# Performance work log

Hardware: AMD Instinct MI355X
Metric: run time of the kernel (lower is better)

Reference implementation:

```python
import jax, jax.numpy as jnp
from jax import lax
import numpy as np
import math

B, LBL, PRED, CIN = 16, 48, 336, 7
L = LBL + PRED
DM, E = 512, 2
DIN, N, DCONV = 2 * DM, 16, 4
DTR = math.ceil(DM / 16)  # 32
TF = 4  # freq='h' time features
EPS = 1e-5


def _ln(x, w, b):
    m = x.mean(-1, keepdims=True)
    v = ((x - m) ** 2).mean(-1, keepdims=True)
    return (x - m) / jnp.sqrt(v + EPS) * w + b


def _silu(x):
    return x * jax.nn.sigmoid(x)


def _token_embed(x, w):
    # Conv1d(c_in, d_model, k=3, padding=1, circular, bias=False). x: (B,L,C), w: (DM,C,3)
    xp = jnp.concatenate([x[:, -1:], x, x[:, :1]], axis=1)  # circular pad along L
    y = lax.conv_general_dilated(xp.transpose(0, 2, 1), w, (1,), 'VALID',
                                 dimension_numbers=('NCH', 'OIH', 'NCH'))
    return y.transpose(0, 2, 1)  # (B,L,DM)


def _selective_scan(u, dt, A, Bm, Cm):
    # u,dt: (B,L,DIN); A: (DIN,N); Bm,Cm: (B,L,N)
    h0 = jnp.zeros((u.shape[0], DIN, N), u.dtype)

    def step(h, inp):
        u_t, dt_t, B_t, C_t = inp  # (B,DIN),(B,DIN),(B,N),(B,N)
        dA = jnp.exp(dt_t[:, :, None] * A)  # (B,DIN,N)
        h = dA * h + (dt_t * u_t)[:, :, None] * B_t[:, None, :]
        y = jnp.einsum('bdn,bn->bd', h, C_t)
        return h, y

    _, ys = lax.scan(step, h0, (u.transpose(1, 0, 2), dt.transpose(1, 0, 2),
                                Bm.transpose(1, 0, 2), Cm.transpose(1, 0, 2)))
    return ys.transpose(1, 0, 2)  # (B,L,DIN)


def _mamba(x, p):
    (in_w, conv_w, conv_b, xproj_w, dtproj_w, dtproj_b, A_log, Dp, out_w) = p
    xz = x @ in_w.T                      # (B,L,2*DIN)
    xin, z = jnp.split(xz, 2, axis=-1)
    # depthwise causal conv1d, kernel DCONV
    xt = jnp.pad(xin.transpose(0, 2, 1), ((0, 0), (0, 0), (DCONV - 1, 0)))
    xc = lax.conv_general_dilated(xt, conv_w, (1,), 'VALID', feature_group_count=DIN,
                                  dimension_numbers=('NCH', 'OIH', 'NCH'))
    xc = _silu((xc + conv_b[None, :, None]).transpose(0, 2, 1))  # (B,L,DIN)
    dbc = xc @ xproj_w.T                 # (B,L,DTR+2N)
    dt_r, Bm, Cm = dbc[..., :DTR], dbc[..., DTR:DTR + N], dbc[..., DTR + N:]
    dt = jax.nn.softplus(dt_r @ dtproj_w.T + dtproj_b)  # (B,L,DIN)
    A = -jnp.exp(A_log)                  # (DIN,N)
    y = _selective_scan(xc, dt, A, Bm, Cm) + xc * Dp
    y = y * _silu(z)
    return y @ out_w.T                   # (B,L,DM)


def _model(x_dec, x_mark_dec, token_w, timef_w, layer_ps, fin_w, fin_b, out_w):
    mean = lax.stop_gradient(x_dec[:, :LBL].mean(1, keepdims=True))
    head = x_dec[:, :LBL] - mean
    std = lax.stop_gradient(jnp.sqrt(head.var(axis=1, keepdims=True) + EPS))
    head = head / std
    xd = jnp.concatenate([head, x_dec[:, LBL:]], axis=1)
    x = _token_embed(xd, token_w) + x_mark_dec @ timef_w.T  # DataEmbedding_wo_pos (eval: no dropout)
    for i in range(E):
        nw, nb = layer_ps[0][i], layer_ps[1][i]
        mp = tuple(layer_ps[j][i] for j in range(2, 11))
        x = x + _mamba(_ln(x, nw, nb), mp)
    x = _ln(x, fin_w, fin_b)
    out = x @ out_w.T
    out = out * std + mean
    return out[:, -PRED:, :]


def setup_inputs() -> dict:
    key = jax.random.key(0)
    ks = jax.random.split(key, 20)
    s = 0.02
    d = {
        'x_enc': jax.random.normal(ks[0], (B, 96, CIN), jnp.float32),
        'x_mark_enc': jax.random.normal(ks[1], (B, 96, TF), jnp.float32),
        'x_dec': jax.random.normal(ks[2], (B, L, CIN), jnp.float32),
        'x_mark_dec': jax.random.normal(ks[3], (B, L, TF), jnp.float32),
        'token_w': jax.random.normal(ks[4], (DM, CIN, 3), jnp.float32) * s,
        'timef_w': jax.random.normal(ks[5], (DM, TF), jnp.float32) * s,
        'norm_w': jnp.ones((E, DM), jnp.float32),
        'norm_b': jnp.zeros((E, DM), jnp.float32),
        'in_proj_w': jax.random.normal(ks[6], (E, 2 * DIN, DM), jnp.float32) * s,
        'conv_w': jax.random.normal(ks[7], (E, DIN, 1, DCONV), jnp.float32) * s,
        'conv_b': jnp.zeros((E, DIN), jnp.float32),
        'xproj_w': jax.random.normal(ks[8], (E, DTR + 2 * N, DIN), jnp.float32) * s,
        'dtproj_w': jax.random.normal(ks[9], (E, DIN, DTR), jnp.float32) * s,
        'dtproj_b': jnp.full((E, DIN), -4.0, jnp.float32),
        'A_log': jnp.tile(jnp.log(jnp.arange(1, N + 1, dtype=jnp.float32)), (E, DIN, 1)),
        'D': jnp.ones((E, DIN), jnp.float32),
        'outproj_w': jax.random.normal(ks[10], (E, DM, DIN), jnp.float32) * s,
        'final_norm_w': jnp.ones((DM,), jnp.float32),
        'final_norm_b': jnp.zeros((DM,), jnp.float32),
        'out_w': jax.random.normal(ks[11], (CIN, DM), jnp.float32) * s,
    }
    return d


def reference(x_enc, x_mark_enc, x_dec, x_mark_dec, token_w, timef_w, norm_w, norm_b,
              in_proj_w, conv_w, conv_b, xproj_w, dtproj_w, dtproj_b, A_log, D,
              outproj_w, final_norm_w, final_norm_b, out_w):
    layer_ps = (norm_w, norm_b, in_proj_w, conv_w, conv_b, xproj_w, dtproj_w,
                dtproj_b, A_log, D, outproj_w)
    return _model(x_dec, x_mark_dec, token_w, timef_w, layer_ps,
                  final_norm_w, final_norm_b, out_w)
```

## Files before the change

### kernel.cpp

```cpp
#include <hip/hip_runtime.h>

#define B_    16
#define LBL_  48
#define PRED_ 336
#define CIN_  7
#define L_    384
#define DM_   512
#define E_    2
#define DIN_  1024
#define N_    16
#define DCONV_ 4
#define DTR_  32
#define TF_   4
#define EPSF  1e-5f
#define NSEG  16
#define SEGL  24
#define SC2   2
#define NCHK  12

typedef unsigned short u16;
typedef __attribute__((ext_vector_type(8))) short short8;
typedef __attribute__((ext_vector_type(4))) float f32x4;

__device__ __forceinline__ float bf2f(u16 u){
  union { float f; unsigned int i; } cv; cv.i = ((unsigned int)u) << 16; return cv.f;
}
__device__ __forceinline__ u16 f2bf(float f){
  union { float f; unsigned int i; } cv; cv.f = f;
  unsigned int x = cv.i;
  unsigned int lsb = (x >> 16) & 1u;
  x += 0x7fffu + lsb;
  return (u16)(x >> 16);
}
__device__ __forceinline__ float lo16(unsigned int v){
  union { float f; unsigned int i; } cv; cv.i = v << 16; return cv.f;
}
__device__ __forceinline__ float hi16(unsigned int v){
  union { float f; unsigned int i; } cv; cv.i = v & 0xffff0000u; return cv.f;
}

#define GLDS(g, l) __builtin_amdgcn_global_load_lds( \
    (const __attribute__((address_space(1))) void*)(g), \
    (__attribute__((address_space(3))) void*)(l), 16, 0, 0)

#define PO_XDEC   0
#define PO_XMARK  43008
#define PO_TOKW   67584
#define PO_TIMEF  78336
#define PO_NORMW  80384
#define PO_NORMB  81408
#define PO_INW    82432
#define PO_CONVW  2179584
#define PO_CONVB  2187776
#define PO_XPROJ  2189824
#define PO_DTW    2320896
#define PO_DTB    2386432
#define PO_ALOG   2388480
#define PO_DP     2421248
#define PO_OUTW   2423296
#define PO_FNW    3471872
#define PO_FNB    3472384
#define PO_HEADW  3472896
#define P_TOTAL   3476480
#define A_X    3476480
#define A_LNB  6622208
#define A_XZ   9767936
#define A_DT   22350848
#define A_DBC  28642304
#define A_XD   29035520
#define A_MEAN 29078528
#define A_STD  29078640
#define A_DBC4 16059392
#define DBC_SL ((size_t)(B_*L_)*64)

struct Ptrs { const void* p[18]; };

__device__ __forceinline__ float wredsum(float s){
  #pragma unroll
  for (int off = 32; off; off >>= 1) s += __shfl_xor(s, off, 64);
  return s;
}

__device__ __forceinline__ void qpowers(float q, float* p){
  float q2 = q*q;
  float q4 = q2*q2;
  float q8 = q4*q4;
  float q3 = q2*q;
  p[0]=q;      p[1]=q2;     p[2]=q3;     p[3]=q4;
  p[4]=q4*q;   p[5]=q4*q2;  p[6]=q4*q3;  p[7]=q8;
  p[8]=q8*q;   p[9]=q8*q2;  p[10]=q8*q3; p[11]=q8*q4;
  p[12]=q8*p[4]; p[13]=q8*p[5]; p[14]=q8*p[6]; p[15]=q8*q8;
}

__device__ __forceinline__ unsigned int xcd_swz(unsigned int bid, unsigned int nwg){
  return (bid & 7u) * (nwg >> 3) + (bid >> 3);
}

__global__ __launch_bounds__(256) void convert_kernel(Ptrs ps, float* __restrict__ dst){
  const int offs[18] = {PO_XDEC, PO_XMARK, PO_TOKW, PO_TIMEF, PO_NORMW, PO_NORMB,
                        PO_INW, PO_CONVW, PO_CONVB, PO_XPROJ, PO_DTW, PO_DTB,
                        PO_ALOG, PO_DP, PO_OUTW, PO_FNW, PO_FNB, PO_HEADW};
  int idx = blockIdx.x * 256 + threadIdx.x;
  if (idx >= P_TOTAL) return;
  int seg = 0;
  #pragma unroll
  for (int s = 1; s < 18; s++) if (idx >= offs[s]) seg = s;
  int off = idx - offs[seg];
  int isbf = (((const u16*)ps.p[4])[0] == 0x3F80u);
  if (seg == 6 || seg == 9 || seg == 10 || seg == 14){
    u16 hv = isbf ? ((const u16*)ps.p[seg])[off]
                  : f2bf(((const float*)ps.p[seg])[off]);
    ((u16*)(dst + offs[seg]))[off] = hv;
  } else {
    float v = isbf ? bf2f(((const u16*)ps.p[seg])[off])
                   : ((const float*)ps.p[seg])[off];
    dst[idx] = v;
  }
}

__global__ __launch_bounds__(64) void prep_kernel(const float* __restrict__ x_dec, float* __restrict__ xd,
                            float* __restrict__ meanv, float* __restrict__ stdv){
  int i = blockIdx.x;
  int b = i / CIN_, c = i % CIN_;
  int lane = threadIdx.x;
  float v0 = (lane < LBL_) ? x_dec[(b*L_+lane)*CIN_+c] : 0.f;
  float m = wredsum(v0) * (1.f/LBL_);
  float dv = (lane < LBL_) ? (v0 - m) : 0.f;
  float sd = sqrtf(wredsum(dv*dv) * (1.f/LBL_) + EPSF);
  if (lane == 0){ meanv[i] = m; stdv[i] = sd; }
  float inv = 1.f / sd;
  #pragma unroll
  for (int t = lane; t < L_; t += 64){
    float v = x_dec[(b*L_+t)*CIN_+c];
    xd[(b*L_+t)*CIN_+c] = (t < LBL_) ? (v - m) * inv : v;
  }
}

__global__ __launch_bounds__(256) void embed_ln_kernel(const float* __restrict__ xd,
      const float* __restrict__ token_w, const float* __restrict__ x_mark,
      const float* __restrict__ timef_w, const float* __restrict__ nw,
      const float* __restrict__ nb, float* __restrict__ x, u16* __restrict__ out){
  int tok = blockIdx.x*4 + (threadIdx.x >> 6);
  int lane = threadIdx.x & 63;
  int t = tok % L_;
  int b = tok / L_;
  int tm1 = (t == 0) ? L_-1 : t-1;
  int tp1 = (t == L_-1) ? 0 : t+1;
  const float* r0 = xd + (b*L_+tm1)*CIN_;
  const float* r1 = xd + (b*L_+t  )*CIN_;
  const float* r2 = xd + (b*L_+tp1)*CIN_;
  const float* mk = x_mark + (b*L_+t)*TF_;
  float a0[CIN_], a1[CIN_], a2[CIN_], mkv[TF_];
  #pragma unroll
  for (int ci = 0; ci < CIN_; ci++){ a0[ci]=r0[ci]; a1[ci]=r1[ci]; a2[ci]=r2[ci]; }
  #pragma unroll
  for (int f = 0; f < TF_; f++) mkv[f] = mk[f];
  float v[8];
  #pragma unroll
  for (int j = 0; j < 8; j++){
    int d = lane*8 + j;
    float acc = 0.f;
    #pragma unroll
    for (int ci = 0; ci < CIN_; ci++){
      const float* w = token_w + (d*CIN_+ci)*3;
      acc += a0[ci]*w[0] + a1[ci]*w[1] + a2[ci]*w[2];
    }
    #pragma unroll
    for (int f = 0; f < TF_; f++)
      acc += mkv[f] * timef_w[d*TF_+f];
    v[j] = acc;
  }
  float* xr = x + (size_t)tok*DM_ + lane*8;
  *(float4*)xr       = (float4){v[0],v[1],v[2],v[3]};
  *(float4*)(xr + 4) = (float4){v[4],v[5],v[6],v[7]};
  float s = (v[0]+v[1])+(v[2]+v[3])+((v[4]+v[5])+(v[6]+v[7]));
  float mean = wredsum(s) * (1.f/DM_);
  float s2 = 0.f;
  #pragma unroll
  for (int j = 0; j < 8; j++){ v[j] -= mean; s2 += v[j]*v[j]; }
  float rstd = rsqrtf(wredsum(s2) * (1.f/DM_) + EPSF);
  const float* wr = nw + lane*8;
  const float* br = nb + lane*8;
  uint4 o; unsigned int* op = (unsigned int*)&o;
  #pragma unroll
  for (int k = 0; k < 4; k++){
    u16 e0 = f2bf(v[2*k]   * rstd * wr[2*k]   + br[2*k]);
    u16 e1 = f2bf(v[2*k+1] * rstd * wr[2*k+1] + br[2*k+1]);
    op[k] = (unsigned int)e0 | ((unsigned int)e1 << 16);
  }
  *(uint4*)(out + (size_t)tok*DM_ + lane*8) = o;
}

__global__ __launch_bounds__(256) void ln_kernel(const float* __restrict__ x,
     const float* __restrict__ w, const float* __restrict__ bias, u16* __restrict__ out){
  int tok = blockIdx.x*4 + (threadIdx.x >> 6);
  int lane = threadIdx.x & 63;
  const float* xr = x + (size_t)tok*DM_ + lane*8;
  float4 a = *(const float4*)xr;
  float4 bq = *(const float4*)(xr + 4);
  float v[8] = {a.x,a.y,a.z,a.w,bq.x,bq.y,bq.z,bq.w};
  float s = (v[0]+v[1])+(v[2]+v[3])+((v[4]+v[5])+(v[6]+v[7]));
  float mean = wredsum(s) * (1.f/DM_);
  float s2 = 0.f;
  #pragma unroll
  for (int j = 0; j < 8; j++){ v[j] -= mean; s2 += v[j]*v[j]; }
  float rstd = rsqrtf(wredsum(s2) * (1.f/DM_) + EPSF);
  const float* wr = w + lane*8;
  const float* br = bias + lane*8;
  uint4 o; unsigned int* op = (unsigned int*)&o;
  #pragma unroll
  for (int k = 0; k < 4; k++){
    u16 e0 = f2bf(v[2*k]   * rstd * wr[2*k]   + br[2*k]);
    u16 e1 = f2bf(v[2*k+1] * rstd * wr[2*k+1] + br[2*k+1]);
    op[k] = (unsigned int)e0 | ((unsigned int)e1 << 16);
  }
  *(uint4*)(out + (size_t)tok*DM_ + lane*8) = o;
}

template<int TN, int ACCUM, int BF16OUT>
__global__ __launch_bounds__(256) void gemm_mfma(const u16* __restrict__ A, const u16* __restrict__ Wt,
    void* __restrict__ C, int M, int N, int K){
  constexpr int WN = TN / 2;
  constexpr int NI = WN / 16;
  __shared__ u16 As[128 * 64];
  __shared__ u16 Ws[TN * 64];
  int tid = threadIdx.x;
  int wv = tid >> 6, lane = tid & 63;
  int wm = (wv & 1) * 64, wn = (wv >> 1) * WN;
  unsigned int gx = gridDim.x;
  unsigned int bid = blockIdx.y * gx + blockIdx.x;
  unsigned int swz = xcd_swz(bid, gx * gridDim.y);
  int m0 = (int)(swz / gx) * 128, n0 = (int)(swz % gx) * TN;
  int la = lane & 15, lk = lane >> 4;
  f32x4 acc[4][NI];
  #pragma unroll
  for (int i = 0; i < 4; i++)
    #pragma unroll
    for (int j = 0; j < NI; j++) acc[i][j] = (f32x4){0.f, 0.f, 0.f, 0.f};
  int sr = lane >> 3;
  int sc = (((lane & 7) ^ (sr & 7)) * 8);
  const u16* Ag = A + (size_t)(m0 + wv*32 + sr) * K + sc;
  u16* Al = As + (wv*32)*64 + lane*8;
  const u16 *Wg; u16 *Wl;
  if constexpr (TN == 128){
    Wg = Wt + (size_t)(n0 + wv*32 + sr) * K + sc;
    Wl = Ws + (wv*32)*64 + lane*8;
  } else {
    Wg = Wt + (size_t)(n0 + wv*16 + sr) * K + sc;
    Wl = Ws + (wv*16)*64 + lane*8;
  }
  for (int k0 = 0; k0 < K; k0 += 64){
    #pragma unroll
    for (int i = 0; i < 4; i++) GLDS(Ag + (size_t)(i*8)*K + k0, Al + i*512);
    if constexpr (TN == 128){
      #pragma unroll
      for (int i = 0; i < 4; i++) GLDS(Wg + (size_t)(i*8)*K + k0, Wl + i*512);
    } else {
      #pragma unroll
      for (int i = 0; i < 2; i++) GLDS(Wg + (size_t)(i*8)*K + k0, Wl + i*512);
    }
    __syncthreads();
    #pragma unroll
    for (int ks = 0; ks < 2; ks++){
      short8 af[4], bfr[NI];
      int ch = (ks*4 + lk) ^ (la & 7);
      #pragma unroll
      for (int mi = 0; mi < 4; mi++) af[mi] = *(const short8*)&As[(wm + mi*16 + la)*64 + ch*8];
      #pragma unroll
      for (int ni = 0; ni < NI; ni++) bfr[ni] = *(const short8*)&Ws[(wn + ni*16 + la)*64 + ch*8];
      #pragma unroll
      for (int mi = 0; mi < 4; mi++)
        #pragma unroll
        for (int ni = 0; ni < NI; ni++)
          acc[mi][ni] = __builtin_amdgcn_mfma_f32_16x16x32_bf16(af[mi], bfr[ni], acc[mi][ni], 0, 0, 0);
    }
    __syncthreads();
  }
  #pragma unroll
  for (int mi = 0; mi < 4; mi++)
    #pragma unroll
    for (int ni = 0; ni < NI; ni++){
      int row = m0 + wm + mi*16 + lk*4;
      int col = n0 + wn + ni*16 + la;
      #pragma unroll
      for (int r = 0; r < 4; r++){
        if constexpr (BF16OUT){
          u16* p = (u16*)C + (size_t)row * N + col;
          p[(size_t)r * N] = f2bf(acc[mi][ni][r]);
        } else {
          float* p = (float*)C + (size_t)row * N + col;
          if (ACCUM) p[(size_t)r * N] += acc[mi][ni][r];
          else       p[(size_t)r * N]  = acc[mi][ni][r];
        }
      }
    }
}

__global__ __launch_bounds__(256) void xproj_mfma(const u16* __restrict__ A, const u16* __restrict__ Wt,
    float* __restrict__ out4){
  __shared__ u16 As[128 * 64];
  __shared__ u16 Ws[64 * 64];
  int tid = threadIdx.x;
  int wv = tid >> 6, lane = tid & 63;
  int wm = (wv & 1) * 64, wn = (wv >> 1) * 32;
  unsigned int gx = gridDim.x;
  unsigned int bid = blockIdx.y * gx + blockIdx.x;
  unsigned int swz = xcd_swz(bid, gx * gridDim.y);
  int m0 = (int)(swz / gx) * 128;
  int kc = (int)(swz % gx);
  int la = lane & 15, lk = lane >> 4;
  f32x4 acc[4][2];
  #pragma unroll
  for (int i = 0; i < 4; i++){ acc[i][0] = (f32x4){0.f,0.f,0.f,0.f}; acc[i][1] = (f32x4){0.f,0.f,0.f,0.f}; }
  int sr = lane >> 3;
  int sc = (((lane & 7) ^ (sr & 7)) * 8);
  const u16* Ag = A + (size_t)(m0 + wv*32 + sr) * DIN_ + kc*256 + sc;
  u16* Al = As + (wv*32)*64 + lane*8;
  const u16* Wg = Wt + (size_t)(wv*16 + sr) * DIN_ + kc*256 + sc;
  u16* Wl = Ws + (wv*16)*64 + lane*8;
  for (int k0 = 0; k0 < 256; k0 += 64){
    #pragma unroll
    for (int i = 0; i < 4; i++) GLDS(Ag + (size_t)(i*8)*DIN_ + k0, Al + i*512);
    #pragma unroll
    for (int i = 0; i < 2; i++) GLDS(Wg + (size_t)(i*8)*DIN_ + k0, Wl + i*512);
    __syncthreads();
    #pragma unroll
    for (int ks = 0; ks < 2; ks++){
      short8 af[4], bfr[2];
      int ch = (ks*4 + lk) ^ (la & 7);
      #pragma unroll
      for (int mi = 0; mi < 4; mi++) af[mi] = *(const short8*)&As[(wm + mi*16 + la)*64 + ch*8];
      #pragma unroll
      for (int ni = 0; ni < 2; ni++) bfr[ni] = *(const short8*)&Ws[(wn + ni*16 + la)*64 + ch*8];
      #pragma unroll
      for (int mi = 0; mi < 4; mi++)
        #pragma unroll
        for (int ni = 0; ni < 2; ni++)
          acc[mi][ni] = __builtin_amdgcn_mfma_f32_16x16x32_bf16(af[mi], bfr[ni], acc[mi][ni], 0, 0, 0);
    }
    __syncthreads();
  }
  #pragma unroll
  for (int mi = 0; mi < 4; mi++)
    #pragma unroll
    for (int ni = 0; ni < 2; ni++){
      int row = m0 + wm + mi*16 + lk*4;
      int col = wn + ni*16 + la;
      #pragma unroll
      for (int r = 0; r < 4; r++)
        out4[((size_t)kc*(B_*L_) + row + r)*64 + col] = acc[mi][ni][r];
    }
}

__global__ __launch_bounds__(256) void dtproj_mfma(const float* __restrict__ dbc4,
    const u16* __restrict__ dtwb, const float* __restrict__ dtb, u16* __restrict__ dt){
  __shared__ u16 As[128 * 32];
  __shared__ u16 Ws[64 * 32];
  int tid = threadIdx.x;
  int wv = tid >> 6, lane = tid & 63;
  int wm = (wv & 1) * 64, wn = (wv >> 1) * 32;
  unsigned int gx = gridDim.x;
  unsigned int bid = blockIdx.y * gx + blockIdx.x;
  unsigned int swz = xcd_swz(bid, gx * gridDim.y);
  int m0 = (int)(swz / gx) * 128, n0 = (int)(swz % gx) * 64;
  int la = lane & 15, lk = lane >> 4;
  int srow = lane >> 2, scol = (lane & 3) * 8;
  #pragma unroll
  for (int i = 0; i < 8; i++){
    int idx = i*512 + tid*2;
    int row = idx >> 5, col = idx & 31;
    const float* p = dbc4 + (size_t)(m0 + row)*64 + col;
    float s0 = 0.f, s1 = 0.f;
    #pragma unroll
    for (int k = 0; k < 4; k++){
      s0 += p[(size_t)k*DBC_SL];
      s1 += p[(size_t)k*DBC_SL + 1];
    }
    *(unsigned int*)&As[row*32 + col] = (unsigned int)f2bf(s0) | ((unsigned int)f2bf(s1) << 16);
  }
  GLDS(dtwb + (size_t)(n0 + wv*16 + srow)*32 + scol, Ws + wv*512 + lane*8);
  __syncthreads();
  short8 af[4], bfr[2];
  #pragma unroll
  for (int mi = 0; mi < 4; mi++) af[mi] = *(const short8*)&As[(wm + mi*16 + la)*32 + lk*8];
  #pragma unroll
  for (int ni = 0; ni < 2; ni++) bfr[ni] = *(const short8*)&Ws[(wn + ni*16 + la)*32 + lk*8];
  #pragma unroll
  for (int mi = 0; mi < 4; mi++)
    #pragma unroll
    for (int ni = 0; ni < 2; ni++){
      f32x4 acc = (f32x4){0.f,0.f,0.f,0.f};
      acc = __builtin_amdgcn_mfma_f32_16x16x32_bf16(af[mi], bfr[ni], acc, 0, 0, 0);
      int row = m0 + wm + mi*16 + lk*4;
      int d   = n0 + wn + ni*16 + la;
      float bias = dtb[d];
      #pragma unroll
      for (int r = 0; r < 4; r++){
        float raw = acc[r] + bias;
        float sp = (raw > 20.f) ? raw : log1pf(__expf(raw));
        dt[(size_t)(row + r)*DIN_ + d] = f2bf(sp);
      }
    }
}

__global__ __launch_bounds__(256) void conv_silu_kernel(const u16* __restrict__ xz,
   const float* __restrict__ cw, const float* __restrict__ cb, u16* __restrict__ xcb){
  int e = blockIdx.x * 256 + threadIdx.x;
  int c8 = (e & (DIN_/8 - 1)) * 8;
  int bt = e >> 7;
  int t  = bt % L_;
  const u16* base = xz + (size_t)bt * (2*DIN_) + c8;
  uint4 tap[4];
  tap[3] = *(const uint4*)base;
  if (t >= 1) tap[2] = *(const uint4*)(base - 1*2*DIN_);
  if (t >= 2) tap[1] = *(const uint4*)(base - 2*2*DIN_);
  if (t >= 3) tap[0] = *(const uint4*)(base - 3*2*DIN_);
  float v[8];
  #pragma unroll
  for (int k = 0; k < 8; k++){
    float4 w = *(const float4*)(cw + (c8 + k)*4);
    float s = cb[c8 + k];
    #pragma unroll
    for (int j = 0; j < 4; j++){
      if (j >= 3 - t){
        const unsigned int* tp = (const unsigned int*)&tap[j];
        float xv = (k & 1) ? hi16(tp[k >> 1]) : lo16(tp[k >> 1]);
        s += xv * ((const float*)&w)[j];
      }
    }
    v[k] = s / (1.f + __expf(-s));
  }
  uint4 o;
  unsigned int* op = (unsigned int*)&o;
  #pragma unroll
  for (int k = 0; k < 4; k++)
    op[k] = (unsigned int)f2bf(v[2*k]) | ((unsigned int)f2bf(v[2*k+1]) << 16);
  *(uint4*)(xcb + (size_t)bt * DIN_ + c8) = o;
}

#define WSTR2 896
__global__ __launch_bounds__(1024, 1) void scan_kernel(
    u16* __restrict__ ub_yb,
    const float* __restrict__ dbc, const u16* __restrict__ xz,
    const u16* __restrict__ dtp,
    const float* __restrict__ A_log, const float* __restrict__ Dp){
  __shared__ float smem[16384];

  int tid = threadIdx.x;
  int lane = tid & 63;
  int seg  = tid >> 6;
  int b = blockIdx.x >> 4;
  int g = blockIdx.x & 15;
  int d = g*64 + lane;
  size_t base = (size_t)b * L_;

  float* wbase = smem + seg * WSTR2;
  float* sbc = wbase;
  float* su  = wbase + 128;
  float* sz  = wbase + 384;
  float* sdt = wbase + 640;

  int st = lane >> 5;
  int j  = lane & 31;

  float A[16];
  #pragma unroll
  for (int n = 0; n < 16; n += 4){
    float4 av = *(const float4*)(A_log + (size_t)d*N_ + n);
    A[n] = -__expf(av.x); A[n+1] = -__expf(av.y); A[n+2] = -__expf(av.z); A[n+3] = -__expf(av.w);
  }
  float Dv = Dp[d];
  bool fastA = true;
  #pragma unroll
  for (int n = 0; n < 16; n++) fastA = fastA && (fabsf(A[n] + (float)(n+1)) < 1e-3f*(n+1));

  float h[16];
  #pragma unroll
  for (int n = 0; n < 16; n++) h[n] = 0.f;

  auto ldc = [&](int c, float& kbc, unsigned int& ku, unsigned int& kz,
                 unsigned int& kt, bool wz){
    size_t tokr = base + seg*SEGL + c*SC2 + st;
    const float* pb = dbc + tokr*64 + 32 + j;
    kbc = (pb[0] + pb[DBC_SL]) + (pb[2*DBC_SL] + pb[3*DBC_SL]);
    ku  = ((const unsigned int*)(ub_yb + tokr*DIN_ + g*64))[j];
    kt  = ((const unsigned int*)(dtp + tokr*DIN_ + g*64))[j];
    if (wz) kz = ((const unsigned int*)(xz + tokr*(2*DIN_) + DIN_ + g*64))[j];
  };
  auto stc = [&](int buf, float kbc, unsigned int ku, unsigned int kz,
                 unsigned int kt, bool wz){
    sbc[buf*64 + st*32 + j] = kbc;
    su [buf*128 + st*64 + 2*j]     = lo16(ku);
    su [buf*128 + st*64 + 2*j + 1] = hi16(ku);
    sdt[buf*128 + st*64 + 2*j]     = lo16(kt);
    sdt[buf*128 + st*64 + 2*j + 1] = hi16(kt);
    if (wz){
      sz[buf*128 + st*64 + 2*j]     = lo16(kz);
      sz[buf*128 + st*64 + 2*j + 1] = hi16(kz);
    }
  };

  float S = 0.f;
  {
    float kbc; unsigned int ku, kz, kt;
    ldc(0, kbc, ku, kz, kt, false);
    stc(0, kbc, ku, kz, kt, false);
    for (int c = 0; c < NCHK; c++){
      int cur = c & 1;
      bool have = (c + 1 < NCHK);
      float nbc; unsigned int nu, nz, nt;
      if (have) ldc(c+1, nbc, nu, nz, nt, false);
      for (int s = 0; s < SC2; s++){
        float dtv = sdt[cur*128 + s*64 + lane];
        float u   = su [cur*128 + s*64 + lane];
        const float* bcrow = sbc + cur*64 + s*32;
        float Bf[16];
        #pragma unroll
        for (int i = 0; i < 16; i += 4){
          float4 bv = *(const float4*)(bcrow + i);
          Bf[i] = bv.x; Bf[i+1] = bv.y; Bf[i+2] = bv.z; Bf[i+3] = bv.w;
        }
        float du = dtv * u;
        S += dtv;
        if (fastA){
          float q = __expf(-dtv);
          float p[16];
          qpowers(q, p);
          #pragma unroll
          for (int n = 0; n < 16; n++) h[n] = p[n] * h[n] + du * Bf[n];
        } else {
          #pragma unroll
          for (int n = 0; n < 16; n++){
            float dA = __expf(dtv * A[n]);
            h[n] = dA * h[n] + du * Bf[n];
          }
        }
      }
      if (have) stc(1 - cur, nbc, nu, nz, nt, false);
    }
  }

  #pragma unroll
  for (int half = 0; half < 2; half++){
    __syncthreads();
    #pragma unroll
    for (int n = 0; n < 8; n++){
      int nn = half*8 + n;
      smem[(n*NSEG + seg)*64 + lane]        = h[nn];
      smem[8192 + (n*NSEG + seg)*64 + lane] = __expf(A[nn] * S);
    }
    __syncthreads();
    float hs[8];
    #pragma unroll
    for (int n = 0; n < 8; n++) hs[n] = 0.f;
    for (int jj = 0; jj < seg; jj++){
      #pragma unroll
      for (int n = 0; n < 8; n++){
        float qh = smem[(n*NSEG + jj)*64 + lane];
        float qP = smem[8192 + (n*NSEG + jj)*64 + lane];
        hs[n] = qh + qP * hs[n];
      }
    }
    #pragma unroll
    for (int n = 0; n < 8; n++) h[half*8 + n] = hs[n];
  }
  __syncthreads();

  {
    float kbc; unsigned int ku, kz, kt;
    ldc(0, kbc, ku, kz, kt, true);
    stc(0, kbc, ku, kz, kt, true);
    for (int c = 0; c < NCHK; c++){
      int cur = c & 1;
      bool have = (c + 1 < NCHK);
      float nbc; unsigned int nu, nz, nt;
      if (have) ldc(c+1, nbc, nu, nz, nt, true);
      for (int s = 0; s < SC2; s++){
        float dtv = sdt[cur*128 + s*64 + lane];
        float u   = su [cur*128 + s*64 + lane];
        float z   = sz [cur*128 + s*64 + lane];
        const float* bcrow = sbc + cur*64 + s*32;
        float Bf[16], Cf[16];
        #pragma unroll
        for (int i = 0; i < 16; i += 4){
          float4 bv = *(const float4*)(bcrow + i);
          float4 cv = *(const float4*)(bcrow + 16 + i);
          Bf[i] = bv.x; Bf[i+1] = bv.y; Bf[i+2] = bv.z; Bf[i+3] = bv.w;
          Cf[i] = cv.x; Cf[i+1] = cv.y; Cf[i+2] = cv.z; Cf[i+3] = cv.w;
        }
        float du = dtv * u;
        float acc = 0.f;
        if (fastA){
          float q = __expf(-dtv);
          float p[16];
          qpowers(q, p);
          #pragma unroll
          for (int n = 0; n < 16; n++){
            h[n] = p[n] * h[n] + du * Bf[n];
            acc += h[n] * Cf[n];
          }
        } else {
          #pragma unroll
          for (int n = 0; n < 16; n++){
            float dA = __expf(dtv * A[n]);
            h[n] = dA * h[n] + du * Bf[n];
            acc += h[n] * Cf[n];
          }
        }
        float y = acc + u * Dv;
        size_t tok = base + seg*SEGL + c*SC2 + s;
        ub_yb[tok*DIN_ + d] = f2bf(y * (z / (1.f + __expf(-z))));
      }
      if (have) stc(1 - cur, nbc, nu, nz, nt, true);
    }
  }
}

__global__ __launch_bounds__(256) void head_kernel(const float* __restrict__ x,
    const float* __restrict__ fw, const float* __restrict__ fb, const float* __restrict__ ow,
    const float* __restrict__ meanv, const float* __restrict__ stdv, void* __restrict__ out,
    const u16* __restrict__ dtype_probe){
  int wav = blockIdx.x*4 + (threadIdx.x >> 6);
  int lane = threadIdx.x & 63;
  if (wav >= B_*PRED_) return;
  int b = wav / PRED_;
  int tt = wav % PRED_;
  int tok = b*L_ + LBL_ + tt;
  const float* xr = x + (size_t)tok*DM_ + lane*8;
  float4 a = *(const float4*)xr;
  float4 bq = *(const float4*)(xr + 4);
  float v[8] = {a.x,a.y,a.z,a.w,bq.x,bq.y,bq.z,bq.w};
  float s = (v[0]+v[1])+(v[2]+v[3])+((v[4]+v[5])+(v[6]+v[7]));
  float mean = wredsum(s) * (1.f/DM_);
  float s2 = 0.f;
  #pragma unroll
  for (int j = 0; j < 8; j++){ v[j] -= mean; s2 += v[j]*v[j]; }
  float rstd = rsqrtf(wredsum(s2) * (1.f/DM_) + EPSF);
  const float* fwr = fw + lane*8;
  const float* fbr = fb + lane*8;
  #pragma unroll
  for (int j = 0; j < 8; j++) v[j] = v[j] * rstd * fwr[j] + fbr[j];
  int isbf = (dtype_probe[0] == 0x3F80u);
  for (int o = 0; o < CIN_; o++){
    const float* owr = ow + (size_t)o*DM_ + lane*8;
    float part = 0.f;
    #pragma unroll
    for (int j = 0; j < 8; j++) part += v[j] * owr[j];
    part = wredsum(part);
    if (lane == 0){
      float res = part * stdv[b*CIN_ + o] + meanv[b*CIN_ + o];
      size_t oidx = (size_t)(b*PRED_ + tt)*CIN_ + o;
      if (isbf) ((u16*)out)[oidx] = f2bf(res);
      else      ((float*)out)[oidx] = res;
    }
  }
}

extern "C" void kernel_launch(void* const* d_in, const int* in_sizes, int n_in,
                              void* d_out, int out_size, void* d_ws, size_t ws_size,
                              hipStream_t stream){
  float* P = (float*)d_ws;

  Ptrs ps;
  for (int i = 0; i < 18; i++) ps.p[i] = d_in[2 + i];

  float* x    = P + A_X;
  u16*   lnxb = (u16*)(P + A_LNB);
  u16*   xcb  = (u16*)(P + A_LNB);
  u16*   xz   = (u16*)(P + A_XZ);
  u16*   dt   = (u16*)(P + A_DT);
  float* dbc4 = P + A_DBC4;
  float* xd   = P + A_XD;
  float* meanv= P + A_MEAN;
  float* stdv = P + A_STD;
  const u16* bwi = (const u16*)(P + PO_INW);
  const u16* bwx = (const u16*)(P + PO_XPROJ);
  const u16* bwd = (const u16*)(P + PO_DTW);
  const u16* bwo = (const u16*)(P + PO_OUTW);

  convert_kernel<<<(P_TOTAL+255)/256, 256, 0, stream>>>(ps, P);
  prep_kernel<<<B_*CIN_, 64, 0, stream>>>(P + PO_XDEC, xd, meanv, stdv);
  embed_ln_kernel<<<(B_*L_)/4, 256, 0, stream>>>(
      xd, P + PO_TOKW, P + PO_XMARK, P + PO_TIMEF,
      P + PO_NORMW, P + PO_NORMB, x, lnxb);

  for (int e = 0; e < E_; e++){
    if (e > 0)
      ln_kernel<<<(B_*L_)/4, 256, 0, stream>>>(x, P + PO_NORMW + e*DM_, P + PO_NORMB + e*DM_, lnxb);
    gemm_mfma<128,0,1><<<dim3((2*DIN_)/128, (B_*L_)/128), 256, 0, stream>>>(
        lnxb, bwi + (size_t)e*2*DIN_*DM_, xz, B_*L_, 2*DIN_, DM_);
    conv_silu_kernel<<<(B_*L_*DIN_)/(256*8), 256, 0, stream>>>(
        xz, P + PO_CONVW + e*DIN_*DCONV_, P + PO_CONVB + e*DIN_, xcb);
    xproj_mfma<<<dim3(4, (B_*L_)/128), 256, 0, stream>>>(
        xcb, bwx + (size_t)e*64*DIN_, dbc4);
    dtproj_mfma<<<dim3(DIN_/64, (B_*L_)/128), 256, 0, stream>>>(
        dbc4, bwd + (size_t)e*DIN_*DTR_, P + PO_DTB + e*DIN_, dt);
    scan_kernel<<<256, 1024, 0, stream>>>(
        xcb, dbc4, xz, dt, P + PO_ALOG + e*DIN_*N_, P + PO_DP + e*DIN_);
    gemm_mfma<64,1,0><<<dim3(DM_/64, (B_*L_)/128), 256, 0, stream>>>(
        xcb, bwo + (size_t)e*DM_*DIN_, x, B_*L_, DM_, DIN_);
  }

  head_kernel<<<(B_*PRED_+3)/4, 256, 0, stream>>>(
      x, P + PO_FNW, P + PO_FNB, P + PO_HEADW, meanv, stdv, d_out, (const u16*)d_in[6]);
}
```

Measured before the change: 414.2 us.

## Fuse in-projection GEMM with causal conv+SiLU and fold prep into embed

Replaces the in_proj GEMM and the separate depthwise conv+SiLU kernel with one kernel. Each block computes a full 384-token by 64-column tile for one batch, stages the bf16 result in LDS and applies the causal conv and SiLU there. The xc half is written straight to xcb and never round-trips through xz. The input-normalisation prep kernel is folded into the embedding kernel, removing a launch and the xd buffer. The trade-offs are a larger LDS tile with lower grid parallelism (512 blocks), redundant per-block statistics computation, and xcb moving into the dt region of the workspace.

```diff
diff --git a/kernel.cpp b/kernel.cpp
--- a/kernel.cpp
+++ b/kernel.cpp
@@ -67,11 +67,11 @@
 #define A_XZ   9767936
 #define A_DT   22350848
 #define A_DBC  28642304
-#define A_XD   29035520
 #define A_MEAN 29078528
 #define A_STD  29078640
 #define A_DBC4 16059392
 #define DBC_SL ((size_t)(B_*L_)*64)
+#define A_XCB_OFF 3145728
 
 struct Ptrs { const void* p[18]; };
 
@@ -118,41 +118,39 @@
   }
 }
 
-__global__ __launch_bounds__(64) void prep_kernel(const float* __restrict__ x_dec, float* __restrict__ xd,
-                            float* __restrict__ meanv, float* __restrict__ stdv){
-  int i = blockIdx.x;
-  int b = i / CIN_, c = i % CIN_;
-  int lane = threadIdx.x;
-  float v0 = (lane < LBL_) ? x_dec[(b*L_+lane)*CIN_+c] : 0.f;
-  float m = wredsum(v0) * (1.f/LBL_);
-  float dv = (lane < LBL_) ? (v0 - m) : 0.f;
-  float sd = sqrtf(wredsum(dv*dv) * (1.f/LBL_) + EPSF);
-  if (lane == 0){ meanv[i] = m; stdv[i] = sd; }
-  float inv = 1.f / sd;
-  #pragma unroll
-  for (int t = lane; t < L_; t += 64){
-    float v = x_dec[(b*L_+t)*CIN_+c];
-    xd[(b*L_+t)*CIN_+c] = (t < LBL_) ? (v - m) * inv : v;
-  }
-}
-
-__global__ __launch_bounds__(256) void embed_ln_kernel(const float* __restrict__ xd,
+__global__ __launch_bounds__(256) void embed_ln_kernel(const float* __restrict__ x_dec,
       const float* __restrict__ token_w, const float* __restrict__ x_mark,
       const float* __restrict__ timef_w, const float* __restrict__ nw,
-      const float* __restrict__ nb, float* __restrict__ x, u16* __restrict__ out){
-  int tok = blockIdx.x*4 + (threadIdx.x >> 6);
+      const float* __restrict__ nb, float* __restrict__ x, u16* __restrict__ out,
+      float* __restrict__ meanv, float* __restrict__ stdv){
+  __shared__ float sm[8], siv[8], ssd[8];
+  int wv = threadIdx.x >> 6;
   int lane = threadIdx.x & 63;
+  int tok = blockIdx.x*4 + wv;
   int t = tok % L_;
   int b = tok / L_;
+  for (int c = wv; c < CIN_; c += 4){
+    float v0 = (lane < LBL_) ? x_dec[(b*L_+lane)*CIN_+c] : 0.f;
+    float m = wredsum(v0) * (1.f/LBL_);
+    float dv = (lane < LBL_) ? (v0 - m) : 0.f;
+    float sd = sqrtf(wredsum(dv*dv) * (1.f/LBL_) + EPSF);
+    if (lane == 0){ sm[c] = m; siv[c] = 1.f/sd; ssd[c] = sd; }
+  }
+  __syncthreads();
+  if ((blockIdx.x % (L_/4)) == 0 && threadIdx.x < CIN_){
+    meanv[b*CIN_ + threadIdx.x] = sm[threadIdx.x];
+    stdv[b*CIN_ + threadIdx.x]  = ssd[threadIdx.x];
+  }
   int tm1 = (t == 0) ? L_-1 : t-1;
   int tp1 = (t == L_-1) ? 0 : t+1;
-  const float* r0 = xd + (b*L_+tm1)*CIN_;
-  const float* r1 = xd + (b*L_+t  )*CIN_;
-  const float* r2 = xd + (b*L_+tp1)*CIN_;
+  auto ldx = [&](int row, int c){
+    float v = x_dec[(b*L_+row)*CIN_+c];
+    return (row < LBL_) ? (v - sm[c]) * siv[c] : v;
+  };
   const float* mk = x_mark + (b*L_+t)*TF_;
   float a0[CIN_], a1[CIN_], a2[CIN_], mkv[TF_];
   #pragma unroll
-  for (int ci = 0; ci < CIN_; ci++){ a0[ci]=r0[ci]; a1[ci]=r1[ci]; a2[ci]=r2[ci]; }
+  for (int ci = 0; ci < CIN_; ci++){ a0[ci]=ldx(tm1,ci); a1[ci]=ldx(t,ci); a2[ci]=ldx(tp1,ci); }
   #pragma unroll
   for (int f = 0; f < TF_; f++) mkv[f] = mk[f];
   float v[8];
@@ -215,6 +213,111 @@
     op[k] = (unsigned int)e0 | ((unsigned int)e1 << 16);
   }
   *(uint4*)(out + (size_t)tok*DM_ + lane*8) = o;
+}
+
+__global__ __launch_bounds__(256) void inproj_conv(const u16* __restrict__ A,
+    const u16* __restrict__ Wt, const float* __restrict__ cw, const float* __restrict__ cb,
+    u16* __restrict__ xz, u16* __restrict__ xcb){
+  __shared__ u16 As[384 * 64];
+  __shared__ u16 Ws[64 * 64];
+  int tid = threadIdx.x;
+  int wv = tid >> 6, lane = tid & 63;
+  unsigned int bid = blockIdx.y * 32 + blockIdx.x;
+  unsigned int swz = xcd_swz(bid, 512);
+  int b  = (int)(swz >> 5);
+  int n0 = (int)(swz & 31) * 64;
+  int m0 = b * L_;
+  int la = lane & 15, lk = lane >> 4;
+  f32x4 acc[6][4];
+  #pragma unroll
+  for (int i = 0; i < 6; i++)
+    #pragma unroll
+    for (int j = 0; j < 4; j++) acc[i][j] = (f32x4){0.f,0.f,0.f,0.f};
+  int sr = lane >> 3;
+  int sc = (((lane & 7) ^ (sr & 7)) * 8);
+  const u16* Ag = A + (size_t)(m0 + wv*96 + sr) * DM_ + sc;
+  u16* Al = As + (wv*96)*64 + lane*8;
+  const u16* Wg = Wt + (size_t)(n0 + wv*16 + sr) * DM_ + sc;
+  u16* Wl = Ws + (wv*16)*64 + lane*8;
+  for (int k0 = 0; k0 < DM_; k0 += 64){
+    #pragma unroll
+    for (int i = 0; i < 12; i++) GLDS(Ag + (size_t)(i*8)*DM_ + k0, Al + i*512);
+    #pragma unroll
+    for (int i = 0; i < 2; i++)  GLDS(Wg + (size_t)(i*8)*DM_ + k0, Wl + i*512);
+    __syncthreads();
+    #pragma unroll
+    for (int ks = 0; ks < 2; ks++){
+      int ch = (ks*4 + lk) ^ (la & 7);
+      short8 af[6], bfr[4];
+      #pragma unroll
+      for (int mi = 0; mi < 6; mi++) af[mi] = *(const short8*)&As[(wv*96 + mi*16 + la)*64 + ch*8];
+      #pragma unroll
+      for (int ni = 0; ni < 4; ni++) bfr[ni] = *(const short8*)&Ws[(ni*16 + la)*64 + ch*8];
+      #pragma unroll
+      for (int mi = 0; mi < 6; mi++)
+        #pragma unroll
+        for (int ni = 0; ni < 4; ni++)
+          acc[mi][ni] = __builtin_amdgcn_mfma_f32_16x16x32_bf16(af[mi], bfr[ni], acc[mi][ni], 0, 0, 0);
+    }
+    __syncthreads();
+  }
+  #pragma unroll
+  for (int mi = 0; mi < 6; mi++)
+    #pragma unroll
+    for (int ni = 0; ni < 4; ni++){
+      int colc = ni*2 + (la >> 3);
+      #pragma unroll
+      for (int r = 0; r < 4; r++){
+        int row = wv*96 + mi*16 + lk*4 + r;
+        As[row*64 + ((colc ^ (row & 7))<<3) + (la & 7)] = f2bf(acc[mi][ni][r]);
+      }
+    }
+  __syncthreads();
+  int c8 = (tid & 7) * 8;
+  int tg = tid >> 3;
+  if (n0 < DIN_){
+    float4 w[8]; float bias[8];
+    #pragma unroll
+    for (int k = 0; k < 8; k++){
+      w[k] = *(const float4*)(cw + (n0 + c8 + k)*4);
+      bias[k] = cb[n0 + c8 + k];
+    }
+    for (int i = 0; i < 12; i++){
+      int t = tg*12 + i;
+      uint4 tap[4];
+      #pragma unroll
+      for (int j = 0; j < 4; j++){
+        int rr = t - 3 + j;
+        if (rr >= 0)
+          tap[j] = *(const uint4*)&As[rr*64 + ((((c8>>3) ^ (rr & 7)))<<3)];
+      }
+      float v[8];
+      #pragma unroll
+      for (int k = 0; k < 8; k++){
+        float s = bias[k];
+        #pragma unroll
+        for (int j = 0; j < 4; j++){
+          if (j >= 3 - t){
+            const unsigned int* tp = (const unsigned int*)&tap[j];
+            float xv = (k & 1) ? hi16(tp[k >> 1]) : lo16(tp[k >> 1]);
+            s += xv * ((const float*)&w[k])[j];
+          }
+        }
+        v[k] = s / (1.f + __expf(-s));
+      }
+      uint4 o; unsigned int* op = (unsigned int*)&o;
+      #pragma unroll
+      for (int k = 0; k < 4; k++)
+        op[k] = (unsigned int)f2bf(v[2*k]) | ((unsigned int)f2bf(v[2*k+1]) << 16);
+      *(uint4*)(xcb + (size_t)(m0 + t)*DIN_ + n0 + c8) = o;
+    }
+  } else {
+    for (int i = 0; i < 12; i++){
+      int t = tg*12 + i;
+      uint4 vq = *(const uint4*)&As[t*64 + ((((c8>>3) ^ (t & 7)))<<3)];
+      *(uint4*)(xz + (size_t)(m0 + t)*(2*DIN_) + n0 + c8) = vq;
+    }
+  }
 }
 
 template<int TN, int ACCUM, int BF16OUT>
@@ -401,41 +504,6 @@
         dt[(size_t)(row + r)*DIN_ + d] = f2bf(sp);
       }
     }
-}
-
-__global__ __launch_bounds__(256) void conv_silu_kernel(const u16* __restrict__ xz,
-   const float* __restrict__ cw, const float* __restrict__ cb, u16* __restrict__ xcb){
-  int e = blockIdx.x * 256 + threadIdx.x;
-  int c8 = (e & (DIN_/8 - 1)) * 8;
-  int bt = e >> 7;
-  int t  = bt % L_;
-  const u16* base = xz + (size_t)bt * (2*DIN_) + c8;
-  uint4 tap[4];
-  tap[3] = *(const uint4*)base;
-  if (t >= 1) tap[2] = *(const uint4*)(base - 1*2*DIN_);
-  if (t >= 2) tap[1] = *(const uint4*)(base - 2*2*DIN_);
-  if (t >= 3) tap[0] = *(const uint4*)(base - 3*2*DIN_);
-  float v[8];
-  #pragma unroll
-  for (int k = 0; k < 8; k++){
-    float4 w = *(const float4*)(cw + (c8 + k)*4);
-    float s = cb[c8 + k];
-    #pragma unroll
-    for (int j = 0; j < 4; j++){
-      if (j >= 3 - t){
-        const unsigned int* tp = (const unsigned int*)&tap[j];
-        float xv = (k & 1) ? hi16(tp[k >> 1]) : lo16(tp[k >> 1]);
-        s += xv * ((const float*)&w)[j];
-      }
-    }
-    v[k] = s / (1.f + __expf(-s));
-  }
-  uint4 o;
-  unsigned int* op = (unsigned int*)&o;
-  #pragma unroll
-  for (int k = 0; k < 4; k++)
-    op[k] = (unsigned int)f2bf(v[2*k]) | ((unsigned int)f2bf(v[2*k+1]) << 16);
-  *(uint4*)(xcb + (size_t)bt * DIN_ + c8) = o;
 }
 
 #define WSTR2 896
@@ -666,11 +734,10 @@
 
   float* x    = P + A_X;
   u16*   lnxb = (u16*)(P + A_LNB);
-  u16*   xcb  = (u16*)(P + A_LNB);
   u16*   xz   = (u16*)(P + A_XZ);
   u16*   dt   = (u16*)(P + A_DT);
+  u16*   xcb  = (u16*)(P + A_DT + A_XCB_OFF);
   float* dbc4 = P + A_DBC4;
-  float* xd   = P + A_XD;
   float* meanv= P + A_MEAN;
   float* stdv = P + A_STD;
   const u16* bwi = (const u16*)(P + PO_INW);
@@ -679,18 +746,16 @@
   const u16* bwo = (const u16*)(P + PO_OUTW);
 
   convert_kernel<<<(P_TOTAL+255)/256, 256, 0, stream>>>(ps, P);
-  prep_kernel<<<B_*CIN_, 64, 0, stream>>>(P + PO_XDEC, xd, meanv, stdv);
   embed_ln_kernel<<<(B_*L_)/4, 256, 0, stream>>>(
-      xd, P + PO_TOKW, P + PO_XMARK, P + PO_TIMEF,
-      P + PO_NORMW, P + PO_NORMB, x, lnxb);
+      P + PO_XDEC, P + PO_TOKW, P + PO_XMARK, P + PO_TIMEF,
+      P + PO_NORMW, P + PO_NORMB, x, lnxb, meanv, stdv);
 
   for (int e = 0; e < E_; e++){
     if (e > 0)
       ln_kernel<<<(B_*L_)/4, 256, 0, stream>>>(x, P + PO_NORMW + e*DM_, P + PO_NORMB + e*DM_, lnxb);
-    gemm_mfma<128,0,1><<<dim3((2*DIN_)/128, (B_*L_)/128), 256, 0, stream>>>(
-        lnxb, bwi + (size_t)e*2*DIN_*DM_, xz, B_*L_, 2*DIN_, DM_);
-    conv_silu_kernel<<<(B_*L_*DIN_)/(256*8), 256, 0, stream>>>(
-        xz, P + PO_CONVW + e*DIN_*DCONV_, P + PO_CONVB + e*DIN_, xcb);
+    inproj_conv<<<dim3(32, 16), 256, 0, stream>>>(
+        lnxb, bwi + (size_t)e*2*DIN_*DM_,
+        P + PO_CONVW + e*DIN_*DCONV_, P + PO_CONVB + e*DIN_, xz, xcb);
     xproj_mfma<<<dim3(4, (B_*L_)/128), 256, 0, stream>>>(
         xcb, bwx + (size_t)e*64*DIN_, dbc4);
     dtproj_mfma<<<dim3(DIN_/64, (B_*L_)/128), 256, 0, stream>>>(
```

Result: faster. 392.8 us (-5.2%).
